# Kernel optimization log

Measured on AMD Instinct MI355X. Metric: run time of the kernel, lower is better.

Reference implementation:

```python
import jax, jax.numpy as jnp
import numpy as np

B, D_IN, D_OUT, E, K, H = 8192, 1024, 1024, 8, 2, 2048


def setup_inputs() -> dict:
    key = jax.random.key(0)
    ks = jax.random.split(key, 7)
    s_in = 1.0 / np.sqrt(D_IN)
    s_h = 1.0 / np.sqrt(H)
    return {
        "x": jax.random.normal(ks[0], (B, D_IN), dtype=jnp.float32),
        "Wg": jax.random.uniform(ks[1], (D_IN, E), minval=-s_in, maxval=s_in, dtype=jnp.float32),
        "bg": jax.random.uniform(ks[2], (E,), minval=-s_in, maxval=s_in, dtype=jnp.float32),
        "W1": jax.random.uniform(ks[3], (E, D_IN, H), minval=-s_in, maxval=s_in, dtype=jnp.float32),
        "b1": jax.random.uniform(ks[4], (E, H), minval=-s_in, maxval=s_in, dtype=jnp.float32),
        "W2": jax.random.uniform(ks[5], (E, H, D_OUT), minval=-s_h, maxval=s_h, dtype=jnp.float32),
        "b2": jax.random.uniform(ks[6], (E, D_OUT), minval=-s_h, maxval=s_h, dtype=jnp.float32),
    }


def reference(x, Wg, bg, W1, b1, W2, b2):
    # gating: linear then top-k -> binary mask (scores are NOT used as weights)
    gate_scores = x @ Wg + bg                      # [B, E]
    _, topk_idx = jax.lax.top_k(gate_scores, K)    # [B, K]
    mask = jax.nn.one_hot(topk_idx, E, dtype=x.dtype).sum(axis=-2)  # [B, E]

    # dense compute of ALL experts (faithful to original module)
    h = jax.nn.relu(jnp.einsum('bi,eih->beh', x, W1) + b1[None])    # [B, E, H]
    expert_out = jnp.einsum('beh,eho->beo', h, W2) + b2[None]       # [B, E, D_OUT]

    # mask to top-k experts and sum over experts
    return jnp.einsum('beo,be->bo', expert_out, mask)               # [B, D_OUT]
```

## Files before the change

kernel.cpp:

```cpp
#include <hip/hip_runtime.h>


#define NTOK 8192
#define DIN  1024
#define DOUT 1024
#define NEXP 8
#define NHID 2048
#define NENT (NTOK * 2)
#define ABLK 64

typedef __bf16 bf16_t;
typedef __bf16 bf16x8 __attribute__((ext_vector_type(8)));
typedef __bf16 bf16x4 __attribute__((ext_vector_type(4)));
typedef float  f32x4  __attribute__((ext_vector_type(4)));

#define AS3(p) ((__attribute__((address_space(3))) void*)(unsigned)(unsigned long long)(p))
#define AS1(p) ((__attribute__((address_space(1))) void*)(unsigned long long)(p))

static __device__ __forceinline__ int imin_(int a, int b) { return a < b ? a : b; }

static __device__ __forceinline__ int xcd_swizzle() {
    int cpx = gridDim.x >> 3;
    return (blockIdx.x & 7) * cpx + (blockIdx.x >> 3);
}

__global__ __launch_bounds__(256) void k_transpose_cvt(
    const float* __restrict__ W, bf16_t* __restrict__ WT, int K_, int N_)
{
    __shared__ float tile[64][65];
    const int tilesK = K_ >> 6, tilesN = N_ >> 6;
    int bid = blockIdx.x;
    int e = bid / (tilesK * tilesN);
    int r = bid % (tilesK * tilesN);
    int tk = (r / tilesN) << 6;
    int tn = (r % tilesN) << 6;
    const float* Wb  = W  + (size_t)e * K_ * N_;
    bf16_t*      WTb = WT + (size_t)e * K_ * N_;
    int lr = threadIdx.x >> 6;
    int lc = threadIdx.x & 63;
#pragma unroll
    for (int i = 0; i < 16; ++i) {
        int row = i * 4 + lr;
        tile[row][lc] = Wb[(size_t)(tk + row) * N_ + tn + lc];
    }
    __syncthreads();
#pragma unroll
    for (int i = 0; i < 16; ++i) {
        int row = i * 4 + lr;
        WTb[(size_t)(tn + row) * K_ + tk + lc] = (bf16_t)tile[lc][row];
    }
}

__global__ __launch_bounds__(256) void k_wgT(
    const float* __restrict__ Wg, float* __restrict__ WgT)
{
    int i = blockIdx.x * 256 + threadIdx.x;
    int d = i >> 3, e = i & 7;
    WgT[e * DIN + d] = Wg[i];
}

__global__ __launch_bounds__(256) void k_gating(
    const float* __restrict__ x, const float* __restrict__ WgT,
    const float* __restrict__ bg, bf16_t* __restrict__ xb,
    int* __restrict__ topk)
{
    int lane = threadIdx.x & 63;
    int tok  = blockIdx.x * 4 + (threadIdx.x >> 6);
    const float* xr  = x  + (size_t)tok * DIN;
    bf16_t*      xbr = xb + (size_t)tok * DIN;

    float4 xv[4];
#pragma unroll
    for (int i = 0; i < 4; ++i) {
        int idx = i * 256 + lane * 4;
        xv[i] = *reinterpret_cast<const float4*>(xr + idx);
        bf16x4 o;
        o[0] = (bf16_t)xv[i].x; o[1] = (bf16_t)xv[i].y;
        o[2] = (bf16_t)xv[i].z; o[3] = (bf16_t)xv[i].w;
        *reinterpret_cast<bf16x4*>(xbr + idx) = o;
    }

    float acc[NEXP];
#pragma unroll
    for (int e = 0; e < NEXP; ++e) {
        const float* we = WgT + (size_t)e * DIN;
        float a = 0.f;
#pragma unroll
        for (int i = 0; i < 4; ++i) {
            int idx = i * 256 + lane * 4;
            float4 w = *reinterpret_cast<const float4*>(we + idx);
            a += xv[i].x * w.x + xv[i].y * w.y + xv[i].z * w.z + xv[i].w * w.w;
        }
        acc[e] = a;
    }

#pragma unroll
    for (int e = 0; e < NEXP; ++e) {
#pragma unroll
        for (int off = 32; off >= 1; off >>= 1) acc[e] += __shfl_xor(acc[e], off);
    }
    if (lane == 0) {
        float s[NEXP];
#pragma unroll
        for (int e = 0; e < NEXP; ++e) s[e] = acc[e] + bg[e];
        int e0 = 0;
        for (int e = 1; e < NEXP; ++e) if (s[e] > s[e0]) e0 = e;
        int e1 = (e0 == 0) ? 1 : 0;
        for (int e = 0; e < NEXP; ++e) if (e != e0 && s[e] > s[e1]) e1 = e;
        topk[2 * tok]     = e0;
        topk[2 * tok + 1] = e1;
    }
}

__global__ __launch_bounds__(256) void k_hist(
    const int* __restrict__ topk, int* __restrict__ bh)
{
    __shared__ int h[NEXP];
    if (threadIdx.x < NEXP) h[threadIdx.x] = 0;
    __syncthreads();
    int i = blockIdx.x * 256 + threadIdx.x;
    atomicAdd(&h[topk[i]], 1);
    __syncthreads();
    if (threadIdx.x < NEXP) bh[blockIdx.x * NEXP + threadIdx.x] = h[threadIdx.x];
}

__global__ void k_scan2(const int* __restrict__ bh, int* __restrict__ counts,
                        int* __restrict__ offsets, int* __restrict__ blockbase)
{
    __shared__ int sc[NEXP], so_[NEXP + 1];
    int t = threadIdx.x;
    if (t < NEXP) {
        int s = 0;
        for (int b = 0; b < ABLK; ++b) s += bh[b * NEXP + t];
        sc[t] = s;
    }
    __syncthreads();
    if (t == 0) {
        int s = 0;
        for (int e = 0; e < NEXP; ++e) { so_[e] = s; s += sc[e]; }
        so_[NEXP] = s;
        for (int e = 0; e <= NEXP; ++e) offsets[e] = so_[e];
        for (int e = 0; e < NEXP; ++e) counts[e] = sc[e];
    }
    __syncthreads();
    if (t < NEXP) {
        int run = so_[t];
        for (int b = 0; b < ABLK; ++b) {
            blockbase[b * NEXP + t] = run;
            run += bh[b * NEXP + t];
        }
    }
}

__global__ __launch_bounds__(256) void k_assign(
    const int* __restrict__ topk, const int* __restrict__ blockbase,
    int* __restrict__ token_ids, int* __restrict__ slot_of)
{
    __shared__ int wcnt[4][NEXP];
    int tid = threadIdx.x, blk = blockIdx.x;
    int i = blk * 256 + tid;
    int e = topk[i];
    int lane = tid & 63, w = tid >> 6;
    unsigned long long ltmask = (1ull << lane) - 1ull;
    int rank_w = 0;
#pragma unroll
    for (int ee = 0; ee < NEXP; ++ee) {
        unsigned long long m = __ballot(e == ee);
        if (ee == e) rank_w = (int)__popcll(m & ltmask);
        if (lane == 0) wcnt[w][ee] = (int)__popcll(m);
    }
    __syncthreads();
    int pre = 0;
    for (int wv = 0; wv < w; ++wv) pre += wcnt[wv][e];
    int s = blockbase[blk * NEXP + e] + pre + rank_w;
    token_ids[s] = i >> 1;
    slot_of[i] = s;
}

__global__ __launch_bounds__(256) void k_gemm1(
    const bf16_t* __restrict__ xb, const bf16_t* __restrict__ w1t,
    const float* __restrict__ b1, bf16_t* __restrict__ hb,
    const int* __restrict__ token_ids, const int* __restrict__ counts,
    const int* __restrict__ offsets)
{
    constexpr int MC = NTOK / 128;
    constexpr int NC = NHID / 128;
    int bid = xcd_swizzle();
    int e  = bid / (MC * NC);
    int r  = bid % (MC * NC);
    int mc = r / NC;
    int nc = r % NC;
    int count = counts[e];
    if (mc * 128 >= count) return;
    int base = offsets[e];

    __shared__ short At[128][32];
    __shared__ short Bt[128][32];

    int t    = threadIdx.x;
    int lane = t & 63;
    int w    = t >> 6;
    int wr   = (w >> 1) * 64;
    int wc   = (w & 1) * 64;

    int r0 = t >> 2;
    int r1 = 64 + r0;
    int c0 = (t & 3) * 8;

    int row0 = imin_(mc * 128 + r0, count - 1);
    int row1 = imin_(mc * 128 + r1, count - 1);
    const bf16_t* a0 = xb + (size_t)token_ids[base + row0] * DIN + c0;
    const bf16_t* a1 = xb + (size_t)token_ids[base + row1] * DIN + c0;
    const bf16_t* wbase = w1t + (size_t)e * NHID * DIN;
    const bf16_t* bp0 = wbase + (size_t)(nc * 128 + r0) * DIN + c0;
    const bf16_t* bp1 = wbase + (size_t)(nc * 128 + r1) * DIN + c0;

    unsigned lds0 = (unsigned)(t & 192) * 16;
    unsigned lds1 = 4096u + lds0;

    f32x4 acc[4][4];
#pragma unroll
    for (int m = 0; m < 4; ++m)
#pragma unroll
        for (int n = 0; n < 4; ++n) acc[m][n] = (f32x4){0.f, 0.f, 0.f, 0.f};

    char* AtB = (char*)&At[0][0];
    char* BtB = (char*)&Bt[0][0];

    for (int k0 = 0; k0 < DIN; k0 += 32) {
        __builtin_amdgcn_global_load_lds(AS1(a0 + k0),  AS3(AtB + lds0), 16, 0, 0);
        __builtin_amdgcn_global_load_lds(AS1(a1 + k0),  AS3(AtB + lds1), 16, 0, 0);
        __builtin_amdgcn_global_load_lds(AS1(bp0 + k0), AS3(BtB + lds0), 16, 0, 0);
        __builtin_amdgcn_global_load_lds(AS1(bp1 + k0), AS3(BtB + lds1), 16, 0, 0);
        __syncthreads();

        bf16x8 af[4], bfv[4];
        int kr = (lane >> 4) * 8;
#pragma unroll
        for (int m = 0; m < 4; ++m)
            af[m] = *reinterpret_cast<const bf16x8*>(&At[wr + m * 16 + (lane & 15)][kr]);
#pragma unroll
        for (int n = 0; n < 4; ++n)
            bfv[n] = *reinterpret_cast<const bf16x8*>(&Bt[wc + n * 16 + (lane & 15)][kr]);
#pragma unroll
        for (int m = 0; m < 4; ++m)
#pragma unroll
            for (int n = 0; n < 4; ++n)
                acc[m][n] = __builtin_amdgcn_mfma_f32_16x16x32_bf16(af[m], bfv[n], acc[m][n], 0, 0, 0);
        __syncthreads();
    }

    int cl = lane & 15;
    int rq = (lane >> 4) * 4;
#pragma unroll
    for (int n = 0; n < 4; ++n) {
        int col  = nc * 128 + wc + n * 16 + cl;
        float bias = b1[e * NHID + col];
#pragma unroll
        for (int m = 0; m < 4; ++m) {
            int rbase = mc * 128 + wr + m * 16 + rq;
#pragma unroll
            for (int q = 0; q < 4; ++q) {
                int gr = rbase + q;
                if (gr < count) {
                    float v = acc[m][n][q] + bias;
                    v = v > 0.f ? v : 0.f;
                    hb[(size_t)(base + gr) * NHID + col] = (bf16_t)v;
                }
            }
        }
    }
}

__global__ __launch_bounds__(256) void k_gemm2(
    const bf16_t* __restrict__ hb, const bf16_t* __restrict__ w2t,
    bf16_t* __restrict__ so,
    const int* __restrict__ counts, const int* __restrict__ offsets)
{
    constexpr int MC = NTOK / 128;
    constexpr int NC = DOUT / 128;
    int bid = xcd_swizzle();
    int e  = bid / (MC * NC);
    int r  = bid % (MC * NC);
    int mc = r / NC;
    int nc = r % NC;
    int count = counts[e];
    if (mc * 128 >= count) return;
    int base = offsets[e];

    __shared__ short At[128][32];
    __shared__ short Bt[128][32];

    int t    = threadIdx.x;
    int lane = t & 63;
    int w    = t >> 6;
    int wr   = (w >> 1) * 64;
    int wc   = (w & 1) * 64;

    int r0 = t >> 2;
    int r1 = 64 + r0;
    int c0 = (t & 3) * 8;

    int row0 = imin_(mc * 128 + r0, count - 1);
    int row1 = imin_(mc * 128 + r1, count - 1);
    const bf16_t* a0 = hb + (size_t)(base + row0) * NHID + c0;
    const bf16_t* a1 = hb + (size_t)(base + row1) * NHID + c0;
    const bf16_t* wbase = w2t + (size_t)e * DOUT * NHID;
    const bf16_t* bp0 = wbase + (size_t)(nc * 128 + r0) * NHID + c0;
    const bf16_t* bp1 = wbase + (size_t)(nc * 128 + r1) * NHID + c0;

    unsigned lds0 = (unsigned)(t & 192) * 16;
    unsigned lds1 = 4096u + lds0;

    f32x4 acc[4][4];
#pragma unroll
    for (int m = 0; m < 4; ++m)
#pragma unroll
        for (int n = 0; n < 4; ++n) acc[m][n] = (f32x4){0.f, 0.f, 0.f, 0.f};

    char* AtB = (char*)&At[0][0];
    char* BtB = (char*)&Bt[0][0];

    for (int k0 = 0; k0 < NHID; k0 += 32) {
        __builtin_amdgcn_global_load_lds(AS1(a0 + k0),  AS3(AtB + lds0), 16, 0, 0);
        __builtin_amdgcn_global_load_lds(AS1(a1 + k0),  AS3(AtB + lds1), 16, 0, 0);
        __builtin_amdgcn_global_load_lds(AS1(bp0 + k0), AS3(BtB + lds0), 16, 0, 0);
        __builtin_amdgcn_global_load_lds(AS1(bp1 + k0), AS3(BtB + lds1), 16, 0, 0);
        __syncthreads();

        bf16x8 af[4], bfv[4];
        int kr = (lane >> 4) * 8;
#pragma unroll
        for (int m = 0; m < 4; ++m)
            af[m] = *reinterpret_cast<const bf16x8*>(&At[wr + m * 16 + (lane & 15)][kr]);
#pragma unroll
        for (int n = 0; n < 4; ++n)
            bfv[n] = *reinterpret_cast<const bf16x8*>(&Bt[wc + n * 16 + (lane & 15)][kr]);
#pragma unroll
        for (int m = 0; m < 4; ++m)
#pragma unroll
            for (int n = 0; n < 4; ++n)
                acc[m][n] = __builtin_amdgcn_mfma_f32_16x16x32_bf16(af[m], bfv[n], acc[m][n], 0, 0, 0);
        __syncthreads();
    }

    int cl = lane & 15;
    int rq = (lane >> 4) * 4;
#pragma unroll
    for (int n = 0; n < 4; ++n) {
        int col = nc * 128 + wc + n * 16 + cl;
#pragma unroll
        for (int m = 0; m < 4; ++m) {
            int rbase = mc * 128 + wr + m * 16 + rq;
#pragma unroll
            for (int q = 0; q < 4; ++q) {
                int gr = rbase + q;
                if (gr < count)
                    so[(size_t)(base + gr) * DOUT + col] = (bf16_t)acc[m][n][q];
            }
        }
    }
}

__global__ __launch_bounds__(256) void k_combine(
    const bf16_t* __restrict__ so, const float* __restrict__ b2,
    const int* __restrict__ topk, const int* __restrict__ slot_of,
    float* __restrict__ out)
{
    int tid = threadIdx.x;
    int tok = blockIdx.x * 2 + (tid >> 7);
    int c0  = (tid & 127) * 8;
    int s0 = slot_of[2 * tok],  s1 = slot_of[2 * tok + 1];
    int e0 = topk[2 * tok],     e1 = topk[2 * tok + 1];
    bf16x8 a = *reinterpret_cast<const bf16x8*>(so + (size_t)s0 * DOUT + c0);
    bf16x8 b = *reinterpret_cast<const bf16x8*>(so + (size_t)s1 * DOUT + c0);
    const float* bb0 = b2 + (size_t)e0 * DOUT + c0;
    const float* bb1 = b2 + (size_t)e1 * DOUT + c0;
    float* op = out + (size_t)tok * DOUT + c0;
    float4 o0, o1;
    o0.x = (float)a[0] + (float)b[0] + bb0[0] + bb1[0];
    o0.y = (float)a[1] + (float)b[1] + bb0[1] + bb1[1];
    o0.z = (float)a[2] + (float)b[2] + bb0[2] + bb1[2];
    o0.w = (float)a[3] + (float)b[3] + bb0[3] + bb1[3];
    o1.x = (float)a[4] + (float)b[4] + bb0[4] + bb1[4];
    o1.y = (float)a[5] + (float)b[5] + bb0[5] + bb1[5];
    o1.z = (float)a[6] + (float)b[6] + bb0[6] + bb1[6];
    o1.w = (float)a[7] + (float)b[7] + bb0[7] + bb1[7];
    *reinterpret_cast<float4*>(op)     = o0;
    *reinterpret_cast<float4*>(op + 4) = o1;
}

extern "C" void kernel_launch(void* const* d_in, const int* in_sizes, int n_in,
                              void* d_out, int out_size, void* d_ws, size_t ws_size,
                              hipStream_t stream)
{
    const float* x  = (const float*)d_in[0];
    const float* Wg = (const float*)d_in[1];
    const float* bg = (const float*)d_in[2];
    const float* W1 = (const float*)d_in[3];
    const float* b1 = (const float*)d_in[4];
    const float* W2 = (const float*)d_in[5];
    const float* b2 = (const float*)d_in[6];
    float* out = (float*)d_out;

    char* ws = (char*)d_ws;
    bf16_t* xb        = (bf16_t*)(ws);
    bf16_t* w1t       = (bf16_t*)(ws + 16777216);
    bf16_t* w2t       = (bf16_t*)(ws + 50331648);
    bf16_t* hb        = (bf16_t*)(ws + 83886080);
    int*    topk      = (int*)(ws + 150994944);
    int*    counts    = (int*)(ws + 151060480);
    int*    offsets   = (int*)(ws + 151060544);
    int*    token_ids = (int*)(ws + 151060608);
    int*    bh        = (int*)(ws + 151126144);
    int*    blockbase = (int*)(ws + 151128192);
    int*    slot_of   = (int*)(ws + 151130240);

    bf16_t* so = (bf16_t*)ws;
    float* wgT = (float*)hb;

    k_wgT<<<(DIN * NEXP) / 256, 256, 0, stream>>>(Wg, wgT);

    k_transpose_cvt<<<NEXP * (DIN / 64) * (NHID / 64), 256, 0, stream>>>(W1, w1t, DIN, NHID);
    k_transpose_cvt<<<NEXP * (NHID / 64) * (DOUT / 64), 256, 0, stream>>>(W2, w2t, NHID, DOUT);

    k_gating<<<NTOK / 4, 256, 0, stream>>>(x, wgT, bg, xb, topk);
    k_hist<<<ABLK, 256, 0, stream>>>(topk, bh);
    k_scan2<<<1, 64, 0, stream>>>(bh, counts, offsets, blockbase);
    k_assign<<<ABLK, 256, 0, stream>>>(topk, blockbase, token_ids, slot_of);

    k_gemm1<<<NEXP * (NTOK / 128) * (NHID / 128), 256, 0, stream>>>(
        xb, w1t, b1, hb, token_ids, counts, offsets);
    k_gemm2<<<NEXP * (NTOK / 128) * (DOUT / 128), 256, 0, stream>>>(
        hb, w2t, so, counts, offsets);
    k_combine<<<NTOK / 2, 256, 0, stream>>>(so, b2, topk, slot_of, out);
}
```

Before: 286.0 us.

## Double-buffer LDS tiles in both expert GEMMs to overlap loads with MFMA

Both grouped GEMM kernels now use two LDS buffers per operand. The next K-tile's global-to-LDS loads are issued before the MFMA work on the current tile, and a single barrier per iteration replaces the old load, wait, compute, wait sequence. The aim is to hide global memory latency behind matrix math. It doubles LDS use per block to 32 KB. If the compiler conservatively waits on all outstanding vector loads before the LDS reads, much of the overlap could be lost.

```diff
diff --git a/kernel.cpp b/kernel.cpp
--- a/kernel.cpp
+++ b/kernel.cpp
@@ -194,8 +194,8 @@
     if (mc * 128 >= count) return;
     int base = offsets[e];
 
-    __shared__ short At[128][32];
-    __shared__ short Bt[128][32];
+    __shared__ short At[2][128][32];
+    __shared__ short Bt[2][128][32];
 
     int t    = threadIdx.x;
     int lane = t & 63;
@@ -224,31 +224,41 @@
 #pragma unroll
         for (int n = 0; n < 4; ++n) acc[m][n] = (f32x4){0.f, 0.f, 0.f, 0.f};
 
-    char* AtB = (char*)&At[0][0];
-    char* BtB = (char*)&Bt[0][0];
-
-    for (int k0 = 0; k0 < DIN; k0 += 32) {
-        __builtin_amdgcn_global_load_lds(AS1(a0 + k0),  AS3(AtB + lds0), 16, 0, 0);
-        __builtin_amdgcn_global_load_lds(AS1(a1 + k0),  AS3(AtB + lds1), 16, 0, 0);
-        __builtin_amdgcn_global_load_lds(AS1(bp0 + k0), AS3(BtB + lds0), 16, 0, 0);
-        __builtin_amdgcn_global_load_lds(AS1(bp1 + k0), AS3(BtB + lds1), 16, 0, 0);
-        __syncthreads();
+    char* AtB = (char*)&At[0][0][0];
+    char* BtB = (char*)&Bt[0][0][0];
+
+#define STAGE1(buf, koff) do {                                                              \
+    __builtin_amdgcn_global_load_lds(AS1(a0  + (koff)), AS3(AtB + (buf) * 8192 + lds0), 16, 0, 0); \
+    __builtin_amdgcn_global_load_lds(AS1(a1  + (koff)), AS3(AtB + (buf) * 8192 + lds1), 16, 0, 0); \
+    __builtin_amdgcn_global_load_lds(AS1(bp0 + (koff)), AS3(BtB + (buf) * 8192 + lds0), 16, 0, 0); \
+    __builtin_amdgcn_global_load_lds(AS1(bp1 + (koff)), AS3(BtB + (buf) * 8192 + lds1), 16, 0, 0); \
+  } while (0)
+
+    STAGE1(0, 0);
+    __syncthreads();
+
+    constexpr int NK = DIN / 32;
+    for (int kt = 0; kt < NK; ++kt) {
+        int cur = kt & 1;
+        if (kt + 1 < NK) STAGE1(cur ^ 1, (kt + 1) * 32);
 
         bf16x8 af[4], bfv[4];
         int kr = (lane >> 4) * 8;
 #pragma unroll
         for (int m = 0; m < 4; ++m)
-            af[m] = *reinterpret_cast<const bf16x8*>(&At[wr + m * 16 + (lane & 15)][kr]);
+            af[m] = *reinterpret_cast<const bf16x8*>(&At[cur][wr + m * 16 + (lane & 15)][kr]);
 #pragma unroll
         for (int n = 0; n < 4; ++n)
-            bfv[n] = *reinterpret_cast<const bf16x8*>(&Bt[wc + n * 16 + (lane & 15)][kr]);
+            bfv[n] = *reinterpret_cast<const bf16x8*>(&Bt[cur][wc + n * 16 + (lane & 15)][kr]);
 #pragma unroll
         for (int m = 0; m < 4; ++m)
 #pragma unroll
             for (int n = 0; n < 4; ++n)
                 acc[m][n] = __builtin_amdgcn_mfma_f32_16x16x32_bf16(af[m], bfv[n], acc[m][n], 0, 0, 0);
+
         __syncthreads();
     }
+#undef STAGE1
 
     int cl = lane & 15;
     int rq = (lane >> 4) * 4;
@@ -288,8 +298,8 @@
     if (mc * 128 >= count) return;
     int base = offsets[e];
 
-    __shared__ short At[128][32];
-    __shared__ short Bt[128][32];
+    __shared__ short At[2][128][32];
+    __shared__ short Bt[2][128][32];
 
     int t    = threadIdx.x;
     int lane = t & 63;
@@ -318,31 +328,41 @@
 #pragma unroll
         for (int n = 0; n < 4; ++n) acc[m][n] = (f32x4){0.f, 0.f, 0.f, 0.f};
 
-    char* AtB = (char*)&At[0][0];
-    char* BtB = (char*)&Bt[0][0];
-
-    for (int k0 = 0; k0 < NHID; k0 += 32) {
-        __builtin_amdgcn_global_load_lds(AS1(a0 + k0),  AS3(AtB + lds0), 16, 0, 0);
-        __builtin_amdgcn_global_load_lds(AS1(a1 + k0),  AS3(AtB + lds1), 16, 0, 0);
-        __builtin_amdgcn_global_load_lds(AS1(bp0 + k0), AS3(BtB + lds0), 16, 0, 0);
-        __builtin_amdgcn_global_load_lds(AS1(bp1 + k0), AS3(BtB + lds1), 16, 0, 0);
-        __syncthreads();
+    char* AtB = (char*)&At[0][0][0];
+    char* BtB = (char*)&Bt[0][0][0];
+
+#define STAGE2(buf, koff) do {                                                              \
+    __builtin_amdgcn_global_load_lds(AS1(a0  + (koff)), AS3(AtB + (buf) * 8192 + lds0), 16, 0, 0); \
+    __builtin_amdgcn_global_load_lds(AS1(a1  + (koff)), AS3(AtB + (buf) * 8192 + lds1), 16, 0, 0); \
+    __builtin_amdgcn_global_load_lds(AS1(bp0 + (koff)), AS3(BtB + (buf) * 8192 + lds0), 16, 0, 0); \
+    __builtin_amdgcn_global_load_lds(AS1(bp1 + (koff)), AS3(BtB + (buf) * 8192 + lds1), 16, 0, 0); \
+  } while (0)
+
+    STAGE2(0, 0);
+    __syncthreads();
+
+    constexpr int NK = NHID / 32;
+    for (int kt = 0; kt < NK; ++kt) {
+        int cur = kt & 1;
+        if (kt + 1 < NK) STAGE2(cur ^ 1, (kt + 1) * 32);
 
         bf16x8 af[4], bfv[4];
         int kr = (lane >> 4) * 8;
 #pragma unroll
         for (int m = 0; m < 4; ++m)
-            af[m] = *reinterpret_cast<const bf16x8*>(&At[wr + m * 16 + (lane & 15)][kr]);
+            af[m] = *reinterpret_cast<const bf16x8*>(&At[cur][wr + m * 16 + (lane & 15)][kr]);
 #pragma unroll
         for (int n = 0; n < 4; ++n)
-            bfv[n] = *reinterpret_cast<const bf16x8*>(&Bt[wc + n * 16 + (lane & 15)][kr]);
+            bfv[n] = *reinterpret_cast<const bf16x8*>(&Bt[cur][wc + n * 16 + (lane & 15)][kr]);
 #pragma unroll
         for (int m = 0; m < 4; ++m)
 #pragma unroll
             for (int n = 0; n < 4; ++n)
                 acc[m][n] = __builtin_amdgcn_mfma_f32_16x16x32_bf16(af[m], bfv[n], acc[m][n], 0, 0, 0);
+
         __syncthreads();
     }
+#undef STAGE2
 
     int cl = lane & 15;
     int rq = (lane >> 4) * 4;
```

Result: slower. 296.7 us (+3.7%).

## Pre-gather routed tokens into contiguous buffer and reuse workspace regions

Applied to the files above, without the earlier changes.

Adds a gather kernel that copies each routed token's bf16 row into an expert-sorted contiguous buffer, so gemm1 loads A tiles with plain strided addressing instead of indirect token_ids lookups. The workspace is re-laid out to alias buffers, with xb/w1t and w2t/xs/so sharing space. To make the aliasing safe, the weight transposes are moved to run just before the GEMM that consumes them. This adds an extra 32MB read/write pass and a kernel launch in exchange for contiguous GEMM loads and a smaller workspace footprint.

```diff
diff --git a/kernel.cpp b/kernel.cpp
--- a/kernel.cpp
+++ b/kernel.cpp
@@ -177,11 +177,22 @@
     slot_of[i] = s;
 }
 
+__global__ __launch_bounds__(256) void k_gather(
+    const bf16_t* __restrict__ xb, const int* __restrict__ token_ids,
+    bf16_t* __restrict__ xs)
+{
+    int tid  = threadIdx.x;
+    int slot = blockIdx.x * 2 + (tid >> 7);
+    int c0   = (tid & 127) * 8;
+    int tok  = token_ids[slot];
+    bf16x8 v = *reinterpret_cast<const bf16x8*>(xb + (size_t)tok * DIN + c0);
+    *reinterpret_cast<bf16x8*>(xs + (size_t)slot * DIN + c0) = v;
+}
+
 __global__ __launch_bounds__(256) void k_gemm1(
-    const bf16_t* __restrict__ xb, const bf16_t* __restrict__ w1t,
+    const bf16_t* __restrict__ xs, const bf16_t* __restrict__ w1t,
     const float* __restrict__ b1, bf16_t* __restrict__ hb,
-    const int* __restrict__ token_ids, const int* __restrict__ counts,
-    const int* __restrict__ offsets)
+    const int* __restrict__ counts, const int* __restrict__ offsets)
 {
     constexpr int MC = NTOK / 128;
     constexpr int NC = NHID / 128;
@@ -209,8 +220,8 @@
 
     int row0 = imin_(mc * 128 + r0, count - 1);
     int row1 = imin_(mc * 128 + r1, count - 1);
-    const bf16_t* a0 = xb + (size_t)token_ids[base + row0] * DIN + c0;
-    const bf16_t* a1 = xb + (size_t)token_ids[base + row1] * DIN + c0;
+    const bf16_t* a0 = xs + (size_t)(base + row0) * DIN + c0;
+    const bf16_t* a1 = xs + (size_t)(base + row1) * DIN + c0;
     const bf16_t* wbase = w1t + (size_t)e * NHID * DIN;
     const bf16_t* bp0 = wbase + (size_t)(nc * 128 + r0) * DIN + c0;
     const bf16_t* bp1 = wbase + (size_t)(nc * 128 + r1) * DIN + c0;
@@ -404,33 +415,37 @@
     float* out = (float*)d_out;
 
     char* ws = (char*)d_ws;
-    bf16_t* xb        = (bf16_t*)(ws);
-    bf16_t* w1t       = (bf16_t*)(ws + 16777216);
-    bf16_t* w2t       = (bf16_t*)(ws + 50331648);
-    bf16_t* hb        = (bf16_t*)(ws + 83886080);
-    int*    topk      = (int*)(ws + 150994944);
-    int*    counts    = (int*)(ws + 151060480);
-    int*    offsets   = (int*)(ws + 151060544);
-    int*    token_ids = (int*)(ws + 151060608);
-    int*    bh        = (int*)(ws + 151126144);
-    int*    blockbase = (int*)(ws + 151128192);
-    int*    slot_of   = (int*)(ws + 151130240);
-
-    bf16_t* so = (bf16_t*)ws;
+    bf16_t* xs        = (bf16_t*)(ws);
+    bf16_t* xb        = (bf16_t*)(ws + 33554432);
+    bf16_t* w1t       = (bf16_t*)(ws + 33554432);
+    bf16_t* hb        = (bf16_t*)(ws + 67108864);
+    int*    topk      = (int*)(ws + 134217728);
+    int*    counts    = (int*)(ws + 134283264);
+    int*    offsets   = (int*)(ws + 134283328);
+    int*    token_ids = (int*)(ws + 134283392);
+    int*    bh        = (int*)(ws + 134348928);
+    int*    blockbase = (int*)(ws + 134350976);
+    int*    slot_of   = (int*)(ws + 134353024);
+    bf16_t* w2t = (bf16_t*)(ws);
+    bf16_t* so  = (bf16_t*)(ws + 33554432);
     float* wgT = (float*)hb;
 
     k_wgT<<<(DIN * NEXP) / 256, 256, 0, stream>>>(Wg, wgT);
-
-    k_transpose_cvt<<<NEXP * (DIN / 64) * (NHID / 64), 256, 0, stream>>>(W1, w1t, DIN, NHID);
-    k_transpose_cvt<<<NEXP * (NHID / 64) * (DOUT / 64), 256, 0, stream>>>(W2, w2t, NHID, DOUT);
 
     k_gating<<<NTOK / 4, 256, 0, stream>>>(x, wgT, bg, xb, topk);
     k_hist<<<ABLK, 256, 0, stream>>>(topk, bh);
     k_scan2<<<1, 64, 0, stream>>>(bh, counts, offsets, blockbase);
     k_assign<<<ABLK, 256, 0, stream>>>(topk, blockbase, token_ids, slot_of);
 
+    k_gather<<<NENT / 2, 256, 0, stream>>>(xb, token_ids, xs);
+
+    k_transpose_cvt<<<NEXP * (DIN / 64) * (NHID / 64), 256, 0, stream>>>(W1, w1t, DIN, NHID);
+
     k_gemm1<<<NEXP * (NTOK / 128) * (NHID / 128), 256, 0, stream>>>(
-        xb, w1t, b1, hb, token_ids, counts, offsets);
+        xs, w1t, b1, hb, counts, offsets);
+
+    k_transpose_cvt<<<NEXP * (NHID / 64) * (DOUT / 64), 256, 0, stream>>>(W2, w2t, NHID, DOUT);
+
     k_gemm2<<<NEXP * (NTOK / 128) * (DOUT / 128), 256, 0, stream>>>(
         hb, w2t, so, counts, offsets);
     k_combine<<<NTOK / 2, 256, 0, stream>>>(so, b2, topk, slot_of, out);
```

Result: slower. 297.0 us (+3.8%).

## Load MFMA fragments directly from global memory with register double buffering

Applied to the files above, without the earlier changes.

Both expert GEMM kernels stop staging A and B tiles through LDS with global_load_lds and two barriers per k-step. Each wave now loads its own bf16x8 fragments straight from global memory into registers and double-buffers two k-steps so loads overlap the MFMAs. This removes LDS traffic and block-level synchronisation. In exchange, data that waves in a block used to share is now fetched separately by each wave (each A row by two waves, each B row by two), uses more registers, and relies on cache for reuse.

```diff
diff --git a/kernel.cpp b/kernel.cpp
--- a/kernel.cpp
+++ b/kernel.cpp
@@ -13,9 +13,6 @@
 typedef __bf16 bf16x8 __attribute__((ext_vector_type(8)));
 typedef __bf16 bf16x4 __attribute__((ext_vector_type(4)));
 typedef float  f32x4  __attribute__((ext_vector_type(4)));
-
-#define AS3(p) ((__attribute__((address_space(3))) void*)(unsigned)(unsigned long long)(p))
-#define AS1(p) ((__attribute__((address_space(1))) void*)(unsigned long long)(p))
 
 static __device__ __forceinline__ int imin_(int a, int b) { return a < b ? a : b; }
 
@@ -177,6 +174,25 @@
     slot_of[i] = s;
 }
 
+
+#define LOADF(A_, B_, K_) do {                                                     \
+    _Pragma("unroll")                                                              \
+    for (int m_ = 0; m_ < 4; ++m_)                                                 \
+        A_[m_] = *reinterpret_cast<const bf16x8*>(aP[m_] + (K_));                  \
+    _Pragma("unroll")                                                              \
+    for (int n_ = 0; n_ < 4; ++n_)                                                 \
+        B_[n_] = *reinterpret_cast<const bf16x8*>(bP[n_] + (K_));                  \
+  } while (0)
+
+#define MFMA16(A_, B_) do {                                                        \
+    _Pragma("unroll")                                                              \
+    for (int m_ = 0; m_ < 4; ++m_)                                                 \
+    { _Pragma("unroll")                                                            \
+      for (int n_ = 0; n_ < 4; ++n_)                                               \
+        acc[m_][n_] = __builtin_amdgcn_mfma_f32_16x16x32_bf16(                     \
+            A_[m_], B_[n_], acc[m_][n_], 0, 0, 0); }                               \
+  } while (0)
+
 __global__ __launch_bounds__(256) void k_gemm1(
     const bf16_t* __restrict__ xb, const bf16_t* __restrict__ w1t,
     const float* __restrict__ b1, bf16_t* __restrict__ hb,
@@ -194,29 +210,26 @@
     if (mc * 128 >= count) return;
     int base = offsets[e];
 
-    __shared__ short At[128][32];
-    __shared__ short Bt[128][32];
-
-    int t    = threadIdx.x;
-    int lane = t & 63;
-    int w    = t >> 6;
+    int lane = threadIdx.x & 63;
+    int w    = threadIdx.x >> 6;
     int wr   = (w >> 1) * 64;
     int wc   = (w & 1) * 64;
-
-    int r0 = t >> 2;
-    int r1 = 64 + r0;
-    int c0 = (t & 3) * 8;
-
-    int row0 = imin_(mc * 128 + r0, count - 1);
-    int row1 = imin_(mc * 128 + r1, count - 1);
-    const bf16_t* a0 = xb + (size_t)token_ids[base + row0] * DIN + c0;
-    const bf16_t* a1 = xb + (size_t)token_ids[base + row1] * DIN + c0;
-    const bf16_t* wbase = w1t + (size_t)e * NHID * DIN;
-    const bf16_t* bp0 = wbase + (size_t)(nc * 128 + r0) * DIN + c0;
-    const bf16_t* bp1 = wbase + (size_t)(nc * 128 + r1) * DIN + c0;
-
-    unsigned lds0 = (unsigned)(t & 192) * 16;
-    unsigned lds1 = 4096u + lds0;
+    int lm   = lane & 15;
+    int kq   = lane >> 4;
+
+    const bf16_t* aP[4];
+    const bf16_t* bP[4];
+    const bf16_t* wbp = w1t + (size_t)e * NHID * DIN + (size_t)kq * 8;
+#pragma unroll
+    for (int m = 0; m < 4; ++m) {
+        int row = imin_(mc * 128 + wr + m * 16 + lm, count - 1);
+        aP[m] = xb + (size_t)token_ids[base + row] * DIN + kq * 8;
+    }
+#pragma unroll
+    for (int n = 0; n < 4; ++n) {
+        int brow = nc * 128 + wc + n * 16 + lm;
+        bP[n] = wbp + (size_t)brow * DIN;
+    }
 
     f32x4 acc[4][4];
 #pragma unroll
@@ -224,37 +237,22 @@
 #pragma unroll
         for (int n = 0; n < 4; ++n) acc[m][n] = (f32x4){0.f, 0.f, 0.f, 0.f};
 
-    char* AtB = (char*)&At[0][0];
-    char* BtB = (char*)&Bt[0][0];
-
-    for (int k0 = 0; k0 < DIN; k0 += 32) {
-        __builtin_amdgcn_global_load_lds(AS1(a0 + k0),  AS3(AtB + lds0), 16, 0, 0);
-        __builtin_amdgcn_global_load_lds(AS1(a1 + k0),  AS3(AtB + lds1), 16, 0, 0);
-        __builtin_amdgcn_global_load_lds(AS1(bp0 + k0), AS3(BtB + lds0), 16, 0, 0);
-        __builtin_amdgcn_global_load_lds(AS1(bp1 + k0), AS3(BtB + lds1), 16, 0, 0);
-        __syncthreads();
-
-        bf16x8 af[4], bfv[4];
-        int kr = (lane >> 4) * 8;
-#pragma unroll
-        for (int m = 0; m < 4; ++m)
-            af[m] = *reinterpret_cast<const bf16x8*>(&At[wr + m * 16 + (lane & 15)][kr]);
-#pragma unroll
-        for (int n = 0; n < 4; ++n)
-            bfv[n] = *reinterpret_cast<const bf16x8*>(&Bt[wc + n * 16 + (lane & 15)][kr]);
-#pragma unroll
-        for (int m = 0; m < 4; ++m)
-#pragma unroll
-            for (int n = 0; n < 4; ++n)
-                acc[m][n] = __builtin_amdgcn_mfma_f32_16x16x32_bf16(af[m], bfv[n], acc[m][n], 0, 0, 0);
-        __syncthreads();
-    }
-
-    int cl = lane & 15;
-    int rq = (lane >> 4) * 4;
+    bf16x8 aE[4], bE[4], aO[4], bO[4];
+    LOADF(aE, bE, 0);
+    LOADF(aO, bO, 32);
+    for (int kt = 0; kt < DIN / 32 - 2; kt += 2) {
+        MFMA16(aE, bE);
+        LOADF(aE, bE, (kt + 2) * 32);
+        MFMA16(aO, bO);
+        LOADF(aO, bO, (kt + 3) * 32);
+    }
+    MFMA16(aE, bE);
+    MFMA16(aO, bO);
+
+    int rq = kq * 4;
 #pragma unroll
     for (int n = 0; n < 4; ++n) {
-        int col  = nc * 128 + wc + n * 16 + cl;
+        int col  = nc * 128 + wc + n * 16 + lm;
         float bias = b1[e * NHID + col];
 #pragma unroll
         for (int m = 0; m < 4; ++m) {
@@ -288,29 +286,26 @@
     if (mc * 128 >= count) return;
     int base = offsets[e];
 
-    __shared__ short At[128][32];
-    __shared__ short Bt[128][32];
-
-    int t    = threadIdx.x;
-    int lane = t & 63;
-    int w    = t >> 6;
+    int lane = threadIdx.x & 63;
+    int w    = threadIdx.x >> 6;
     int wr   = (w >> 1) * 64;
     int wc   = (w & 1) * 64;
-
-    int r0 = t >> 2;
-    int r1 = 64 + r0;
-    int c0 = (t & 3) * 8;
-
-    int row0 = imin_(mc * 128 + r0, count - 1);
-    int row1 = imin_(mc * 128 + r1, count - 1);
-    const bf16_t* a0 = hb + (size_t)(base + row0) * NHID + c0;
-    const bf16_t* a1 = hb + (size_t)(base + row1) * NHID + c0;
-    const bf16_t* wbase = w2t + (size_t)e * DOUT * NHID;
-    const bf16_t* bp0 = wbase + (size_t)(nc * 128 + r0) * NHID + c0;
-    const bf16_t* bp1 = wbase + (size_t)(nc * 128 + r1) * NHID + c0;
-
-    unsigned lds0 = (unsigned)(t & 192) * 16;
-    unsigned lds1 = 4096u + lds0;
+    int lm   = lane & 15;
+    int kq   = lane >> 4;
+
+    const bf16_t* aP[4];
+    const bf16_t* bP[4];
+    const bf16_t* wbp = w2t + (size_t)e * DOUT * NHID + (size_t)kq * 8;
+#pragma unroll
+    for (int m = 0; m < 4; ++m) {
+        int row = imin_(mc * 128 + wr + m * 16 + lm, count - 1);
+        aP[m] = hb + (size_t)(base + row) * NHID + kq * 8;
+    }
+#pragma unroll
+    for (int n = 0; n < 4; ++n) {
+        int brow = nc * 128 + wc + n * 16 + lm;
+        bP[n] = wbp + (size_t)brow * NHID;
+    }
 
     f32x4 acc[4][4];
 #pragma unroll
@@ -318,37 +313,22 @@
 #pragma unroll
         for (int n = 0; n < 4; ++n) acc[m][n] = (f32x4){0.f, 0.f, 0.f, 0.f};
 
-    char* AtB = (char*)&At[0][0];
-    char* BtB = (char*)&Bt[0][0];
-
-    for (int k0 = 0; k0 < NHID; k0 += 32) {
-        __builtin_amdgcn_global_load_lds(AS1(a0 + k0),  AS3(AtB + lds0), 16, 0, 0);
-        __builtin_amdgcn_global_load_lds(AS1(a1 + k0),  AS3(AtB + lds1), 16, 0, 0);
-        __builtin_amdgcn_global_load_lds(AS1(bp0 + k0), AS3(BtB + lds0), 16, 0, 0);
-        __builtin_amdgcn_global_load_lds(AS1(bp1 + k0), AS3(BtB + lds1), 16, 0, 0);
-        __syncthreads();
-
-        bf16x8 af[4], bfv[4];
-        int kr = (lane >> 4) * 8;
-#pragma unroll
-        for (int m = 0; m < 4; ++m)
-            af[m] = *reinterpret_cast<const bf16x8*>(&At[wr + m * 16 + (lane & 15)][kr]);
-#pragma unroll
-        for (int n = 0; n < 4; ++n)
-            bfv[n] = *reinterpret_cast<const bf16x8*>(&Bt[wc + n * 16 + (lane & 15)][kr]);
-#pragma unroll
-        for (int m = 0; m < 4; ++m)
-#pragma unroll
-            for (int n = 0; n < 4; ++n)
-                acc[m][n] = __builtin_amdgcn_mfma_f32_16x16x32_bf16(af[m], bfv[n], acc[m][n], 0, 0, 0);
-        __syncthreads();
-    }
-
-    int cl = lane & 15;
-    int rq = (lane >> 4) * 4;
+    bf16x8 aE[4], bE[4], aO[4], bO[4];
+    LOADF(aE, bE, 0);
+    LOADF(aO, bO, 32);
+    for (int kt = 0; kt < NHID / 32 - 2; kt += 2) {
+        MFMA16(aE, bE);
+        LOADF(aE, bE, (kt + 2) * 32);
+        MFMA16(aO, bO);
+        LOADF(aO, bO, (kt + 3) * 32);
+    }
+    MFMA16(aE, bE);
+    MFMA16(aO, bO);
+
+    int rq = kq * 4;
 #pragma unroll
     for (int n = 0; n < 4; ++n) {
-        int col = nc * 128 + wc + n * 16 + cl;
+        int col = nc * 128 + wc + n * 16 + lm;
 #pragma unroll
         for (int m = 0; m < 4; ++m) {
             int rbase = mc * 128 + wr + m * 16 + rq;
```

New measurement: 639.2 us. +123.5%, slower.
